# Optimization experiments

Hardware: AMD Instinct MI355X
Metric: run time of the kernel (lower is better)

Reference implementation:

```python
import jax, jax.numpy as jnp
import numpy as np

C, H, P = 128, 4, 8  # d_model, n_heads, n_points (n_levels=1)
D = C // H


def setup_inputs() -> dict:
    key = jax.random.key(0)
    ks = jax.random.split(key, 14)
    B, Y, X = 2, 200, 200
    N = Y * X
    s = 0.05
    inp = {
        "query": jax.random.normal(ks[0], (B, N, C), jnp.float32),
        "query_pos": jax.random.normal(ks[1], (B, N, C), jnp.float32),
        # MSDeformAttn params
        "Wv": jax.random.normal(ks[2], (C, C), jnp.float32) * s,
        "bv": jnp.zeros((C,), jnp.float32),
        "Woff": jax.random.normal(ks[3], (C, H * P * 2), jnp.float32) * s,
        "boff": jax.random.normal(ks[4], (H * P * 2,), jnp.float32) * s,
        "Wattn": jax.random.normal(ks[5], (C, H * P), jnp.float32) * s,
        "battn": jnp.zeros((H * P,), jnp.float32),
        "Wout1": jax.random.normal(ks[6], (C, C), jnp.float32) * s,  # MSDeformAttn.output_proj
        "bout1": jnp.zeros((C,), jnp.float32),
        "Wout2": jax.random.normal(ks[7], (C, C), jnp.float32) * s,  # wrapper output_proj
        "bout2": jnp.zeros((C,), jnp.float32),
        "Y": Y,
        "X": X,
    }
    return inp


def _deform_attn(q, v_in, Wv, bv, Woff, boff, Wattn, battn, Wout1, bout1, Y, X):
    B, N, _ = q.shape
    # reference points: grid centers, stacked (y, x) normalized (as in source)
    ref_y = (jnp.arange(Y, dtype=jnp.float32) + 0.5) / Y
    ref_x = (jnp.arange(X, dtype=jnp.float32) + 0.5) / X
    ry, rx = jnp.meshgrid(ref_y, ref_x, indexing="ij")
    ref = jnp.stack([ry.reshape(-1), rx.reshape(-1)], -1)  # (N, 2)

    value = (v_in @ Wv + bv).reshape(B, Y, X, H, D).transpose(0, 3, 1, 2, 4)  # (B,H,Y,X,D)
    off = (q @ Woff + boff).reshape(B, N, H, P, 2)
    attn = jax.nn.softmax((q @ Wattn + battn).reshape(B, N, H, P), axis=-1)

    # offset normalizer = (W, H) = (X, Y); loc = ref + off/norm  (faithful to source)
    norm = jnp.array([X, Y], jnp.float32)
    loc = ref[None, :, None, None, :] + off / norm  # (B,N,H,P,2)

    # grid_sample bilinear, align_corners=False, zero padding; channel 0 = x, 1 = y
    gx = loc[..., 0] * X - 0.5
    gy = loc[..., 1] * Y - 0.5
    x0 = jnp.floor(gx)
    y0 = jnp.floor(gy)
    wx1 = gx - x0
    wy1 = gy - y0
    x0i = x0.astype(jnp.int32)
    y0i = y0.astype(jnp.int32)

    b_idx = jnp.arange(B)[:, None, None, None]
    h_idx = jnp.arange(H)[None, None, :, None]

    def gather(yi, xi, w):
        valid = (yi >= 0) & (yi < Y) & (xi >= 0) & (xi < X)
        yc = jnp.clip(yi, 0, Y - 1)
        xc = jnp.clip(xi, 0, X - 1)
        v = value[b_idx, h_idx, yc, xc]  # (B,N,H,P,D)
        return v * (w * valid)[..., None]

    sampled = (
        gather(y0i, x0i, (1 - wy1) * (1 - wx1))
        + gather(y0i, x0i + 1, (1 - wy1) * wx1)
        + gather(y0i + 1, x0i, wy1 * (1 - wx1))
        + gather(y0i + 1, x0i + 1, wy1 * wx1)
    )
    out = (sampled * attn[..., None]).sum(axis=3).reshape(B, N, C)
    return out @ Wout1 + bout1


def reference(query, query_pos, Wv, bv, Woff, boff, Wattn, battn, Wout1, bout1, Wout2, bout2, Y, X):
    residual = query
    q = query + query_pos
    out = _deform_attn(q, q, Wv, bv, Woff, boff, Wattn, battn, Wout1, bout1, Y, X)
    out = out @ Wout2 + bout2  # wrapper output_proj; dropout in eval mode = identity
    return out + residual
```

## Files before the change

### kernel.cpp

```cpp
#include <hip/hip_runtime.h>
#include <hip/hip_bf16.h>
#include <hip/hip_fp16.h>

#define BQ 2
#define YY 200
#define XX 200
#define NQ 40000
#define CC 128
#define MTOT 80000
#define NCOL 224
#define NTILES 5000

typedef __attribute__((ext_vector_type(8))) short short8;
typedef __attribute__((ext_vector_type(4))) short short4v;
typedef __attribute__((ext_vector_type(4))) float f32x4;

static __device__ __forceinline__ unsigned short f2bf(float f) {
    union { float f; unsigned int u; } v; v.f = f;
    unsigned int r = v.u + 0x7FFF + ((v.u >> 16) & 1);
    return (unsigned short)(r >> 16);
}
static __device__ __forceinline__ unsigned short f2bf_hw(float f) {
    __hip_bfloat16 h = __float2bfloat16(f);
    unsigned short s;
    __builtin_memcpy(&s, &h, 2);
    return s;
}
static __device__ __forceinline__ __half2 u2h2(unsigned int u) {
    __half2 h; __builtin_memcpy(&h, &u, 4); return h;
}
static __device__ __forceinline__ unsigned int h22u(__half2 h) {
    unsigned int u; __builtin_memcpy(&u, &h, 4); return u;
}
static __device__ __forceinline__ short h2s(__half h) {
    short s; __builtin_memcpy(&s, &h, 2); return s;
}

__global__ void prep_wcat(const float* __restrict__ Wv, const float* __restrict__ Woff,
                          const float* __restrict__ Wattn, unsigned short* __restrict__ WcatT) {
    int idx = blockIdx.x * 256 + threadIdx.x;
    if (idx >= NCOL * CC) return;
    int c = idx >> 7, k = idx & 127;
    float w = (c < 128) ? Wv[k * 128 + c]
            : (c < 192) ? Woff[k * 64 + (c - 128)]
                        : Wattn[k * 32 + (c - 192)];
    WcatT[c * 128 + k] = f2bf(w);
}

__global__ void prep_w12(const float* __restrict__ Wout1, const float* __restrict__ Wout2,
                         const float* __restrict__ bout1, const float* __restrict__ bout2,
                         unsigned short* __restrict__ W12T, float* __restrict__ b12) {
    int idx = blockIdx.x * 256 + threadIdx.x;
    int c = idx >> 7, k = idx & 127;
    float s = 0.f;
    for (int j = 0; j < 128; ++j) s += Wout1[k * 128 + j] * Wout2[j * 128 + c];
    W12T[c * 128 + k] = f2bf(s);
    if (k == 0) {
        float t = bout2[c];
        for (int j = 0; j < 128; ++j) t += bout1[j] * Wout2[j * 128 + c];
        b12[c] = t;
    }
}

__global__ __launch_bounds__(256) void qsum_kernel(const float* __restrict__ query,
                                                   const float* __restrict__ qpos,
                                                   unsigned short* __restrict__ qbf) {
    const size_t total = (size_t)MTOT * CC / 8;
    for (size_t c = (size_t)blockIdx.x * 256 + threadIdx.x; c < total;
         c += (size_t)gridDim.x * 256) {
        const float4* a = (const float4*)(query + c * 8);
        const float4* b = (const float4*)(qpos + c * 8);
        float4 a0 = a[0], a1 = a[1], b0 = b[0], b1 = b[1];
        short8 w;
        w[0] = (short)f2bf_hw(a0.x + b0.x); w[1] = (short)f2bf_hw(a0.y + b0.y);
        w[2] = (short)f2bf_hw(a0.z + b0.z); w[3] = (short)f2bf_hw(a0.w + b0.w);
        w[4] = (short)f2bf_hw(a1.x + b1.x); w[5] = (short)f2bf_hw(a1.y + b1.y);
        w[6] = (short)f2bf_hw(a1.z + b1.z); w[7] = (short)f2bf_hw(a1.w + b1.w);
        *(short8*)(qbf + c * 8) = w;
    }
}

__global__ __launch_bounds__(256, 2) void g1_kernel(
    const unsigned short* __restrict__ qbf, const unsigned short* __restrict__ WcatT,
    const float* __restrict__ bv, const float* __restrict__ boff, const float* __restrict__ battn,
    unsigned short* __restrict__ value_h, float* __restrict__ off_out, float* __restrict__ logits_out)
{
    const int tid = threadIdx.x;
    const int group = blockIdx.x >> 8;
    const int gblk = blockIdx.x & 255;
    const int lane = tid & 63;
    const int arow = lane & 15, kq = lane >> 4;
    const int wid = gblk * 4 + (tid >> 6);
    const int tg0 = group * 4;
    const int NT = (group == 3) ? 2 : 4;

    short8 bf[4][4];
#pragma unroll
    for (int t = 0; t < 4; ++t) {
        if (t < NT) {
#pragma unroll
            for (int ks = 0; ks < 4; ++ks)
                bf[t][ks] = *(const short8*)(WcatT + (size_t)((tg0 + t) * 16 + arow) * 128 + ks * 32 + kq * 8);
        }
    }

    f32x4 biasv[4];
#pragma unroll
    for (int t = 0; t < 4; ++t) {
        if (t < NT) {
            const float* bp = (group < 2) ? (bv + (tg0 + t) * 16 + kq * 4)
                            : (group == 2) ? (boff + (tg0 + t - 8) * 16 + kq * 4)
                                           : (battn + (tg0 + t - 12) * 16 + kq * 4);
            float4 b4 = *(const float4*)bp;
            biasv[t] = (f32x4){b4.x, b4.y, b4.z, b4.w};
        }
    }

    for (int tile = wid; tile < NTILES; tile += 1024) {
        const char* pa = (const char*)qbf + (size_t)(tile * 16 + arow) * 256 + kq * 16;
        short8 af[4];
#pragma unroll
        for (int ks = 0; ks < 4; ++ks) af[ks] = *(const short8*)(pa + ks * 64);

        f32x4 acc[4];
#pragma unroll
        for (int t = 0; t < 4; ++t) acc[t] = biasv[t];

#pragma unroll
        for (int ks = 0; ks < 4; ++ks) {
#pragma unroll
            for (int t = 0; t < 4; ++t) {
                if (t < NT)
                    acc[t] = __builtin_amdgcn_mfma_f32_16x16x32_bf16(bf[t][ks], af[ks], acc[t], 0, 0, 0);
            }
        }

        const int row = tile * 16 + arow;
        if (group < 2) {
#pragma unroll
            for (int t = 0; t < 4; ++t) {
                short4v pv;
                pv[0] = h2s(__float2half(acc[t][0])); pv[1] = h2s(__float2half(acc[t][1]));
                pv[2] = h2s(__float2half(acc[t][2])); pv[3] = h2s(__float2half(acc[t][3]));
                *(short4v*)(value_h + (size_t)row * 128 + (tg0 + t) * 16 + kq * 4) = pv;
            }
        } else if (group == 2) {
#pragma unroll
            for (int t = 0; t < 4; ++t) {
                float4 o = make_float4(acc[t][0], acc[t][1], acc[t][2], acc[t][3]);
                *(float4*)(off_out + (size_t)row * 64 + (tg0 + t - 8) * 16 + kq * 4) = o;
            }
        } else {
#pragma unroll
            for (int t = 0; t < 2; ++t) {
                float4 o = make_float4(acc[t][0], acc[t][1], acc[t][2], acc[t][3]);
                *(float4*)(logits_out + (size_t)row * 32 + (tg0 + t - 12) * 16 + kq * 4) = o;
            }
        }
    }
}

__global__ __launch_bounds__(256) void sample_kernel(
    const unsigned short* __restrict__ value_h, const float* __restrict__ off_in,
    const float* __restrict__ logits, unsigned short* __restrict__ sampled)
{
    __shared__ int4 SA[8][33];
    __shared__ int4 SW[8][33];

    const int tid = threadIdx.x;
    const int qi = tid >> 5;
    const int lane = tid & 31;
    const int r = blockIdx.x * 8 + qi;
    const int b = (r >= NQ) ? 1 : 0;
    const int n = r - b * NQ;
    const int yq = n / XX, xq = n - yq * XX;

    {
        float lg = logits[(size_t)r * 32 + lane];
        float m = lg;
        m = fmaxf(m, __shfl_xor(m, 1));
        m = fmaxf(m, __shfl_xor(m, 2));
        m = fmaxf(m, __shfl_xor(m, 4));
        float e = __expf(lg - m);
        float s = e;
        s += __shfl_xor(s, 1);
        s += __shfl_xor(s, 2);
        s += __shfl_xor(s, 4);
        float aw = e / s;

        float2 o = ((const float2*)(off_in + (size_t)r * 64))[lane];
        float gx = (float)yq + o.x;
        float gy = (float)xq + o.y;
        float fx = floorf(gx), fy = floorf(gy);
        int x0 = (int)fx, y0 = (int)fy;
        float wx1 = gx - fx, wy1 = gy - fy;
        float vx0 = ((unsigned)x0 < XX) ? 1.f : 0.f;
        float vx1 = ((unsigned)(x0 + 1) < XX) ? 1.f : 0.f;
        float vy0 = ((unsigned)y0 < YY) ? 1.f : 0.f;
        float vy1 = ((unsigned)(y0 + 1) < YY) ? 1.f : 0.f;
        int x0c = min(max(x0, 0), XX - 1);
        int x1c = min(max(x0 + 1, 0), XX - 1);
        int y0c = min(max(y0, 0), YY - 1);
        int y1c = min(max(y0 + 1, 0), YY - 1);
        int hb = (lane >> 3) * 64;
        int rowA = y0c * XX, rowB = y1c * XX;
        int4 addrs;
        addrs.x = (rowA + x0c) * 256 + hb;
        addrs.y = (rowA + x1c) * 256 + hb;
        addrs.z = (rowB + x0c) * 256 + hb;
        addrs.w = (rowB + x1c) * 256 + hb;

        float wxa = (1.f - wx1) * vx0;
        float wxb = wx1 * vx1;
        float wya = aw * (1.f - wy1) * vy0;
        float wyb = aw * wy1 * vy1;
        int4 wts;
        wts.x = (int)h22u(__float2half2_rn(wxa * wya));
        wts.y = (int)h22u(__float2half2_rn(wxb * wya));
        wts.z = (int)h22u(__float2half2_rn(wxa * wyb));
        wts.w = (int)h22u(__float2half2_rn(wxb * wyb));

        const int slot = (lane & 7) * 4 + (lane >> 3);
        SA[qi][slot] = addrs;
        SW[qi][slot] = wts;
    }
    __syncthreads();

    const char* vb = (const char*)(value_h + (size_t)b * NQ * 128);
    const int h = lane >> 3, oc = lane & 7;
    const int cb = oc * 8;

    __half2 accA0 = __float2half2_rn(0.f), accA1 = __float2half2_rn(0.f);
    __half2 accB0 = __float2half2_rn(0.f), accB1 = __float2half2_rn(0.f);

#pragma unroll
    for (int p = 0; p < 8; ++p) {
        const int slot = p * 4 + h;
        int4 ai = SA[qi][slot];
        int4 wi = SW[qi][slot];

        uint2 u00 = *(const uint2*)(vb + ai.x + cb);
        uint2 u01 = *(const uint2*)(vb + ai.y + cb);
        uint2 u10 = *(const uint2*)(vb + ai.z + cb);
        uint2 u11 = *(const uint2*)(vb + ai.w + cb);

        __half2 w00 = u2h2((unsigned int)wi.x);
        __half2 w01 = u2h2((unsigned int)wi.y);
        __half2 w10 = u2h2((unsigned int)wi.z);
        __half2 w11 = u2h2((unsigned int)wi.w);

        accA0 = __hfma2(w00, u2h2(u00.x), accA0);
        accA1 = __hfma2(w00, u2h2(u00.y), accA1);
        accA0 = __hfma2(w01, u2h2(u01.x), accA0);
        accA1 = __hfma2(w01, u2h2(u01.y), accA1);
        accB0 = __hfma2(w10, u2h2(u10.x), accB0);
        accB1 = __hfma2(w10, u2h2(u10.y), accB1);
        accB0 = __hfma2(w11, u2h2(u11.x), accB0);
        accB1 = __hfma2(w11, u2h2(u11.y), accB1);
    }

    float c0 = __low2float(accA0) + __low2float(accB0);
    float c1 = __high2float(accA0) + __high2float(accB0);
    float c2 = __low2float(accA1) + __low2float(accB1);
    float c3 = __high2float(accA1) + __high2float(accB1);
    uint2 packed;
    packed.x = ((unsigned int)f2bf(c1) << 16) | (unsigned int)f2bf(c0);
    packed.y = ((unsigned int)f2bf(c3) << 16) | (unsigned int)f2bf(c2);
    *(uint2*)((char*)(sampled + (size_t)r * 128) + h * 64 + cb) = packed;
}

__global__ __launch_bounds__(256, 2) void g2_kernel(
    const unsigned short* __restrict__ sampled, const unsigned short* __restrict__ W12T,
    const float* __restrict__ b12, const float* __restrict__ query, float* __restrict__ out)
{
    const int tid = threadIdx.x;
    const int group = blockIdx.x >> 9;
    const int gblk = blockIdx.x & 511;
    const int lane = tid & 63;
    const int arow = lane & 15, kq = lane >> 4;
    const int wid = gblk * 4 + (tid >> 6);
    const int tg0 = group * 4;

    short8 bf[4][4];
#pragma unroll
    for (int t = 0; t < 4; ++t)
#pragma unroll
        for (int ks = 0; ks < 4; ++ks)
            bf[t][ks] = *(const short8*)(W12T + (size_t)((tg0 + t) * 16 + arow) * 128 + ks * 32 + kq * 8);

    f32x4 biasv[4];
#pragma unroll
    for (int t = 0; t < 4; ++t) {
        float4 b4 = *(const float4*)(b12 + (tg0 + t) * 16 + kq * 4);
        biasv[t] = (f32x4){b4.x, b4.y, b4.z, b4.w};
    }

    for (int tile = wid; tile < NTILES; tile += 2048) {
        const char* pa = (const char*)sampled + (size_t)(tile * 16 + arow) * 256 + kq * 16;
        short8 af[4];
#pragma unroll
        for (int ks = 0; ks < 4; ++ks) af[ks] = *(const short8*)(pa + ks * 64);

        f32x4 acc[4];
#pragma unroll
        for (int t = 0; t < 4; ++t) acc[t] = biasv[t];

#pragma unroll
        for (int ks = 0; ks < 4; ++ks)
#pragma unroll
            for (int t = 0; t < 4; ++t)
                acc[t] = __builtin_amdgcn_mfma_f32_16x16x32_bf16(bf[t][ks], af[ks], acc[t], 0, 0, 0);

        const int row = tile * 16 + arow;
#pragma unroll
        for (int t = 0; t < 4; ++t) {
            size_t idx = (size_t)row * 128 + (tg0 + t) * 16 + kq * 4;
            float4 q4 = *(const float4*)(query + idx);
            float4 o = make_float4(acc[t][0] + q4.x, acc[t][1] + q4.y,
                                   acc[t][2] + q4.z, acc[t][3] + q4.w);
            *(float4*)(out + idx) = o;
        }
    }
}

extern "C" void kernel_launch(void* const* d_in, const int* in_sizes, int n_in,
                              void* d_out, int out_size, void* d_ws, size_t ws_size,
                              hipStream_t stream) {
    const float* query = (const float*)d_in[0];
    const float* qpos  = (const float*)d_in[1];
    const float* Wv    = (const float*)d_in[2];
    const float* bv    = (const float*)d_in[3];
    const float* Woff  = (const float*)d_in[4];
    const float* boff  = (const float*)d_in[5];
    const float* Wattn = (const float*)d_in[6];
    const float* battn = (const float*)d_in[7];
    const float* Wout1 = (const float*)d_in[8];
    const float* bout1 = (const float*)d_in[9];
    const float* Wout2 = (const float*)d_in[10];
    const float* bout2 = (const float*)d_in[11];
    float* out = (float*)d_out;

    char* ws = (char*)d_ws;
    unsigned short* value_h  = (unsigned short*)(ws);
    float*          off_buf  = (float*)(ws + 20480000);
    float*          logits   = (float*)(ws + 40960000);
    unsigned short* sampled  = (unsigned short*)(ws + 51200000);
    unsigned short* WcatT    = (unsigned short*)(ws + 71680000);
    unsigned short* W12T     = (unsigned short*)(ws + 71680000 + 57344);
    float*          b12      = (float*)(ws + 71680000 + 57344 + 32768);

    unsigned short* qbf = sampled;

    prep_wcat<<<112, 256, 0, stream>>>(Wv, Woff, Wattn, WcatT);
    prep_w12<<<64, 256, 0, stream>>>(Wout1, Wout2, bout1, bout2, W12T, b12);
    qsum_kernel<<<2048, 256, 0, stream>>>(query, qpos, qbf);
    g1_kernel<<<1024, 256, 0, stream>>>(qbf, WcatT, bv, boff, battn,
                                        value_h, off_buf, logits);
    sample_kernel<<<MTOT / 8, 256, 0, stream>>>(value_h, off_buf, logits, sampled);
    g2_kernel<<<1024, 256, 0, stream>>>(sampled, W12T, b12, query, out);
}
```

Before: 124.2 us.

## Restructure bilinear sampling gathers into 16-byte loads split by corner row

The sampling kernel's lane mapping changes: each lane now handles one y-row of the bilinear corners (two corners) over 8 channels with 16-byte loads, instead of four corners over 4 channels with 8-byte loads. All gathers are issued up front into register arrays before the FMAs, and partial sums from the two y-rows are combined with a cross-lane shuffle. This halves the number of gather instructions and raises memory-level parallelism. In exchange it costs more registers, adds shuffles, and pads the shared arrays to a different stride.

```diff
diff --git a/kernel.cpp b/kernel.cpp
--- a/kernel.cpp
+++ b/kernel.cpp
@@ -164,8 +164,8 @@
     const unsigned short* __restrict__ value_h, const float* __restrict__ off_in,
     const float* __restrict__ logits, unsigned short* __restrict__ sampled)
 {
-    __shared__ int4 SA[8][33];
-    __shared__ int4 SW[8][33];
+    __shared__ int4 SA[8][36];
+    __shared__ int4 SW[8][36];
 
     const int tid = threadIdx.x;
     const int qi = tid >> 5;
@@ -227,46 +227,54 @@
     __syncthreads();
 
     const char* vb = (const char*)(value_h + (size_t)b * NQ * 128);
-    const int h = lane >> 3, oc = lane & 7;
-    const int cb = oc * 8;
-
-    __half2 accA0 = __float2half2_rn(0.f), accA1 = __float2half2_rn(0.f);
-    __half2 accB0 = __float2half2_rn(0.f), accB1 = __float2half2_rn(0.f);
-
+    const int h = lane >> 3, yc = (lane >> 2) & 1, quad = lane & 3;
+    const int cb = quad * 16;
+
+    int2 a[8];
+#pragma unroll
+    for (int p = 0; p < 8; ++p)
+        a[p] = *(const int2*)((const char*)&SA[qi][p * 4 + h] + yc * 8);
+
+    uint4 d0[8], d1[8];
 #pragma unroll
     for (int p = 0; p < 8; ++p) {
-        const int slot = p * 4 + h;
-        int4 ai = SA[qi][slot];
-        int4 wi = SW[qi][slot];
-
-        uint2 u00 = *(const uint2*)(vb + ai.x + cb);
-        uint2 u01 = *(const uint2*)(vb + ai.y + cb);
-        uint2 u10 = *(const uint2*)(vb + ai.z + cb);
-        uint2 u11 = *(const uint2*)(vb + ai.w + cb);
-
-        __half2 w00 = u2h2((unsigned int)wi.x);
-        __half2 w01 = u2h2((unsigned int)wi.y);
-        __half2 w10 = u2h2((unsigned int)wi.z);
-        __half2 w11 = u2h2((unsigned int)wi.w);
-
-        accA0 = __hfma2(w00, u2h2(u00.x), accA0);
-        accA1 = __hfma2(w00, u2h2(u00.y), accA1);
-        accA0 = __hfma2(w01, u2h2(u01.x), accA0);
-        accA1 = __hfma2(w01, u2h2(u01.y), accA1);
-        accB0 = __hfma2(w10, u2h2(u10.x), accB0);
-        accB1 = __hfma2(w10, u2h2(u10.y), accB1);
-        accB0 = __hfma2(w11, u2h2(u11.x), accB0);
-        accB1 = __hfma2(w11, u2h2(u11.y), accB1);
-    }
-
-    float c0 = __low2float(accA0) + __low2float(accB0);
-    float c1 = __high2float(accA0) + __high2float(accB0);
-    float c2 = __low2float(accA1) + __low2float(accB1);
-    float c3 = __high2float(accA1) + __high2float(accB1);
+        d0[p] = *(const uint4*)(vb + a[p].x + cb);
+        d1[p] = *(const uint4*)(vb + a[p].y + cb);
+    }
+
+    int2 w[8];
+#pragma unroll
+    for (int p = 0; p < 8; ++p)
+        w[p] = *(const int2*)((const char*)&SW[qi][p * 4 + h] + yc * 8);
+
+    __half2 acc0 = __float2half2_rn(0.f), acc1 = __float2half2_rn(0.f);
+    __half2 acc2 = __float2half2_rn(0.f), acc3 = __float2half2_rn(0.f);
+
+#pragma unroll
+    for (int p = 0; p < 8; ++p) {
+        __half2 wa = u2h2((unsigned int)w[p].x);
+        __half2 wb = u2h2((unsigned int)w[p].y);
+        acc0 = __hfma2(wa, u2h2(d0[p].x), acc0);
+        acc1 = __hfma2(wa, u2h2(d0[p].y), acc1);
+        acc2 = __hfma2(wa, u2h2(d0[p].z), acc2);
+        acc3 = __hfma2(wa, u2h2(d0[p].w), acc3);
+        acc0 = __hfma2(wb, u2h2(d1[p].x), acc0);
+        acc1 = __hfma2(wb, u2h2(d1[p].y), acc1);
+        acc2 = __hfma2(wb, u2h2(d1[p].z), acc2);
+        acc3 = __hfma2(wb, u2h2(d1[p].w), acc3);
+    }
+
+    acc0 = __hadd2(acc0, u2h2((unsigned int)__shfl_xor((int)h22u(acc0), 4)));
+    acc1 = __hadd2(acc1, u2h2((unsigned int)__shfl_xor((int)h22u(acc1), 4)));
+    acc2 = __hadd2(acc2, u2h2((unsigned int)__shfl_xor((int)h22u(acc2), 4)));
+    acc3 = __hadd2(acc3, u2h2((unsigned int)__shfl_xor((int)h22u(acc3), 4)));
+
+    __half2 pa = (yc == 0) ? acc0 : acc2;
+    __half2 pb = (yc == 0) ? acc1 : acc3;
     uint2 packed;
-    packed.x = ((unsigned int)f2bf(c1) << 16) | (unsigned int)f2bf(c0);
-    packed.y = ((unsigned int)f2bf(c3) << 16) | (unsigned int)f2bf(c2);
-    *(uint2*)((char*)(sampled + (size_t)r * 128) + h * 64 + cb) = packed;
+    packed.x = ((unsigned int)f2bf(__high2float(pa)) << 16) | (unsigned int)f2bf(__low2float(pa));
+    packed.y = ((unsigned int)f2bf(__high2float(pb)) << 16) | (unsigned int)f2bf(__low2float(pb));
+    *(uint2*)((char*)(sampled + (size_t)r * 128) + h * 64 + cb + yc * 8) = packed;
 }
 
 __global__ __launch_bounds__(256, 2) void g2_kernel(
```

New measurement: 113.0 us. 9.1% less time.
